# Kernel tuning notes

Measured on AMD Instinct MI355X. Metric: run time of the kernel, lower is better.

Reference implementation:

```python
import jax, jax.numpy as jnp
import numpy as np

DECAY = 0.9
BETA_OBS = 1.0
BETA_STATE = 1.0

N_OBS = 20000
N_STATES = 1024
N_ACTIONS = 64
STATE_DIM = 256
RFD = 2048


def setup_inputs() -> dict:
    key = jax.random.key(0)
    ks = jax.random.split(key, 7)
    Q = jax.random.normal(ks[0], (STATE_DIM, N_STATES), dtype=jnp.float32) / np.sqrt(STATE_DIM).astype(np.float32)
    V = jax.random.normal(ks[1], (STATE_DIM, N_ACTIONS), dtype=jnp.float32) / np.sqrt(STATE_DIM).astype(np.float32)
    W = jax.random.normal(ks[2], (RFD, STATE_DIM), dtype=jnp.float32)
    M_re = jax.random.normal(ks[3], (RFD, N_OBS), dtype=jnp.float32)
    M_im = jax.random.normal(ks[4], (RFD, N_OBS), dtype=jnp.float32)
    obs = jax.random.uniform(ks[5], (N_OBS,), dtype=jnp.float32)
    action = jax.random.uniform(ks[6], (N_ACTIONS,), dtype=jnp.float32)
    return {"Q": Q, "V": V, "W": W, "M_re": M_re, "M_im": M_im, "obs": obs, "action": action}


def reference(Q, V, W, M_re, M_im, obs, action):
    # One fused POCML step: memory write (decayed outer product), state
    # rotation via complex random-feature phase, clean_up (state-kernel
    # softmax retrieval), and obs retrieval from memory.
    D = W.shape[0]  # random_feature_dim
    M = M_re + 1j * M_im                       # [D, n_obs] complex64
    obs_c = obs.astype(jnp.complex64)
    # get_state_from_memory
    state0 = M @ obs_c                         # [D]
    # update_memory: M *= decay; M += outer(state, obs)
    M_new = DECAY * M + jnp.outer(state0, obs_c)
    # update_state: v = V @ action; phi_v = exp(1j * W @ v); state *= phi_v
    v = V @ action                             # [state_dim]
    phi_v = jnp.exp(1j * (W @ v))              # [D] complex64
    state1 = state0 * phi_v
    # clean_up: phi_Q = exp(1j * W @ Q), weights = softmax(beta*sim(phi_Q.T, state))
    phi_Q = jnp.exp(1j * (W @ Q))              # [D, n_states]
    score = BETA_STATE * (phi_Q.T @ jnp.conj(state1)).real / D  # [n_states]
    weights = jax.nn.softmax(score)
    state2 = phi_Q @ weights.astype(jnp.complex64)              # [D]
    # get_obs_from_memory: softmax(beta_obs * sim(M.T, state))
    obs_score = BETA_OBS * (M_new.T @ jnp.conj(state2)).real / D  # [n_obs]
    return jax.nn.softmax(obs_score)
```

## Files before the change

kernel.cpp:

```cpp
#include <hip/hip_runtime.h>
#include <math.h>

#define N_OBS    20000
#define N_OBS4   5000
#define N_STATES 1024
#define N_ACT    64
#define SDIM     256
#define RFD      2048
#define DECAY    0.9f

typedef float v4f __attribute__((ext_vector_type(4)));

__device__ __forceinline__ v4f ntload4(const float* p) {
    return __builtin_nontemporal_load((const v4f*)p);
}

#define OFF_SCORE  0
#define OFF_OBSACC 1024
#define ZERO_CNT   (OFF_OBSACC + N_OBS)
#define OFF_S0RE   21024
#define OFF_S0IM   23072
#define OFF_S1RE   25120
#define OFF_S1IM   27168
#define OFF_S2RE   29216
#define OFF_S2IM   31264
#define OFF_WTS    33312
#define OFF_VWS    34336
#define OFF_COSQ   34816
#define OFF_SINQ   (OFF_COSQ + RFD*N_STATES)
#define OFF_P0RE   (OFF_SINQ + RFD*N_STATES)
#define OFF_P0IM   (OFF_P0RE + 5*RFD)
#define WS_FLOATS  (OFF_P0IM + 5*RFD)

#define NB_GEMM   512
#define NB_STATE0 (5 * RFD)
#define NB_FUSED  (NB_GEMM + 1 + NB_STATE0)

__global__ __launch_bounds__(256) void k_fused(
    const float* __restrict__ Mre, const float* __restrict__ Mim,
    const float* __restrict__ obs,
    const float* __restrict__ W, const float* __restrict__ Q,
    const float* __restrict__ V, const float* __restrict__ action,
    float* __restrict__ cosQ, float* __restrict__ sinQ,
    float* __restrict__ p0re, float* __restrict__ p0im,
    float* __restrict__ vout)
{
    const int b = blockIdx.x;
    const int tid = threadIdx.x;

    if (b < NB_GEMM) {
        __shared__ float As[16][65];
        __shared__ float Bs[16][64];
        const int tx = tid & 15;
        const int ty = tid >> 4;
        const int m0 = (b >> 4) * 64;
        const int n0 = (b & 15) * 64;
        float c[4][4] = {};
        for (int k0 = 0; k0 < SDIM; k0 += 16) {
            {
                int k = tid & 15, mb = tid >> 4;
                #pragma unroll
                for (int j = 0; j < 4; j++)
                    As[k][mb + 16*j] = W[(size_t)(m0 + mb + 16*j) * SDIM + k0 + k];
            }
            {
                int n = tid & 63, kb = tid >> 6;
                #pragma unroll
                for (int j = 0; j < 4; j++)
                    Bs[kb + 4*j][n] = Q[(size_t)(k0 + kb + 4*j) * N_STATES + n0 + n];
            }
            __syncthreads();
            #pragma unroll
            for (int kk = 0; kk < 16; kk++) {
                float a[4], bb[4];
                #pragma unroll
                for (int i = 0; i < 4; i++) a[i] = As[kk][ty*4 + i];
                #pragma unroll
                for (int j = 0; j < 4; j++) bb[j] = Bs[kk][tx*4 + j];
                #pragma unroll
                for (int i = 0; i < 4; i++)
                    #pragma unroll
                    for (int j = 0; j < 4; j++)
                        c[i][j] += a[i] * bb[j];
            }
            __syncthreads();
        }
        #pragma unroll
        for (int i = 0; i < 4; i++) {
            int d = m0 + ty*4 + i;
            #pragma unroll
            for (int j = 0; j < 4; j++) {
                int s = n0 + tx*4 + j;
                float sn, cs;
                sincosf(c[i][j], &sn, &cs);
                cosQ[(size_t)d * N_STATES + s] = cs;
                sinQ[(size_t)d * N_STATES + s] = sn;
            }
        }
    } else if (b == NB_GEMM) {
        float acc = 0.f;
        for (int a = 0; a < N_ACT; a++) acc += V[tid * N_ACT + a] * action[a];
        vout[tid] = acc;
    } else {
        const int bb = b - (NB_GEMM + 1);
        const int d = bb / 5;
        const int seg = bb - d * 5;
        const float* mr = Mre + (size_t)d * N_OBS;
        const float* mi = Mim + (size_t)d * N_OBS;
        const float4* ob = (const float4*)obs;
        float ar[4] = {}, ai[4] = {};
        #pragma unroll
        for (int it = 0; it < 4; ++it) {
            int i = seg * 1024 + it * 256 + tid;
            bool ok = i < N_OBS4;
            int ic = ok ? i : 0;
            float4 o = ok ? ob[ic] : make_float4(0.f, 0.f, 0.f, 0.f);
            v4f a = ntload4(mr + 4 * (size_t)ic);
            v4f m = ntload4(mi + 4 * (size_t)ic);
            ar[it] += a.x*o.x + a.y*o.y + a.z*o.z + a.w*o.w;
            ai[it] += m.x*o.x + m.y*o.y + m.z*o.z + m.w*o.w;
        }
        float arr = (ar[0] + ar[1]) + (ar[2] + ar[3]);
        float aii = (ai[0] + ai[1]) + (ai[2] + ai[3]);
        #pragma unroll
        for (int off = 32; off > 0; off >>= 1) {
            arr += __shfl_down(arr, off);
            aii += __shfl_down(aii, off);
        }
        __shared__ float pr[4], pi[4];
        const int wave = tid >> 6, lane = tid & 63;
        if (lane == 0) { pr[wave] = arr; pi[wave] = aii; }
        __syncthreads();
        if (tid == 0) {
            p0re[seg * RFD + d] = pr[0] + pr[1] + pr[2] + pr[3];
            p0im[seg * RFD + d] = pi[0] + pi[1] + pi[2] + pi[3];
        }
    }
}

__global__ __launch_bounds__(256) void k_state1(
    const float* __restrict__ W, const float* __restrict__ vws,
    const float* __restrict__ p0re, const float* __restrict__ p0im,
    float* __restrict__ s0re, float* __restrict__ s0im,
    float* __restrict__ s1re, float* __restrict__ s1im)
{
    const int tid = threadIdx.x;
    const int w = tid >> 6, l = tid & 63;
    const int d = blockIdx.x * 4 + w;
    float4 wv = ((const float4*)(W + (size_t)d * SDIM))[l];
    float4 vv = ((const float4*)vws)[l];
    float th = wv.x*vv.x + wv.y*vv.y + wv.z*vv.z + wv.w*vv.w;
    #pragma unroll
    for (int off = 32; off > 0; off >>= 1) th += __shfl_down(th, off);
    if (l == 0) {
        float re = 0.f, im = 0.f;
        #pragma unroll
        for (int s = 0; s < 5; s++) {
            re += p0re[s * RFD + d];
            im += p0im[s * RFD + d];
        }
        s0re[d] = re; s0im[d] = im;
        float sn, cs;
        sincosf(th, &sn, &cs);
        s1re[d] = re * cs - im * sn;
        s1im[d] = re * sn + im * cs;
    }
}

__global__ __launch_bounds__(256) void k_score(
    const float* __restrict__ cosQ, const float* __restrict__ sinQ,
    const float* __restrict__ s1re, const float* __restrict__ s1im,
    float* __restrict__ score)
{
    const int s = blockIdx.x * 256 + threadIdx.x;
    const int d0 = blockIdx.y * 32;
    float acc = 0.f;
    #pragma unroll 4
    for (int j = 0; j < 32; j++) {
        int d = d0 + j;
        acc += cosQ[(size_t)d * N_STATES + s] * s1re[d]
             + sinQ[(size_t)d * N_STATES + s] * s1im[d];
    }
    atomicAdd(&score[s], acc);
}

__global__ __launch_bounds__(256) void k_softmax_w(
    const float* __restrict__ score, float* __restrict__ wts)
{
    __shared__ float red[256];
    const int tid = threadIdx.x;
    const float scale = 1.f / (float)RFD;
    float4 v = ((const float4*)score)[tid];
    v.x *= scale; v.y *= scale; v.z *= scale; v.w *= scale;
    float mx = fmaxf(fmaxf(v.x, v.y), fmaxf(v.z, v.w));
    red[tid] = mx; __syncthreads();
    for (int s = 128; s > 0; s >>= 1) {
        if (tid < s) red[tid] = fmaxf(red[tid], red[tid+s]);
        __syncthreads();
    }
    mx = red[0]; __syncthreads();
    float4 e;
    e.x = expf(v.x - mx); e.y = expf(v.y - mx);
    e.z = expf(v.z - mx); e.w = expf(v.w - mx);
    red[tid] = e.x + e.y + e.z + e.w; __syncthreads();
    for (int s = 128; s > 0; s >>= 1) {
        if (tid < s) red[tid] += red[tid+s];
        __syncthreads();
    }
    const float inv = 1.f / red[0];
    e.x *= inv; e.y *= inv; e.z *= inv; e.w *= inv;
    ((float4*)wts)[tid] = e;
}

__global__ __launch_bounds__(256) void k_state2(
    const float* __restrict__ cosQ, const float* __restrict__ sinQ,
    const float* __restrict__ wts,
    float* __restrict__ s2re, float* __restrict__ s2im)
{
    __shared__ float r1[256], r2[256];
    const int d = blockIdx.x, tid = threadIdx.x;
    float4 w = ((const float4*)wts)[tid];
    float4 a = ((const float4*)(cosQ + (size_t)d * N_STATES))[tid];
    float4 b = ((const float4*)(sinQ + (size_t)d * N_STATES))[tid];
    r1[tid] = a.x*w.x + a.y*w.y + a.z*w.z + a.w*w.w;
    r2[tid] = b.x*w.x + b.y*w.y + b.z*w.z + b.w*w.w;
    __syncthreads();
    for (int s = 128; s > 0; s >>= 1) {
        if (tid < s) { r1[tid] += r1[tid+s]; r2[tid] += r2[tid+s]; }
        __syncthreads();
    }
    if (tid == 0) { s2re[d] = r1[0]; s2im[d] = r2[0]; }
}

__global__ __launch_bounds__(256) void k_obs_acc(
    const float* __restrict__ Mre, const float* __restrict__ Mim,
    const float* __restrict__ s2re, const float* __restrict__ s2im,
    float* __restrict__ obs_acc)
{
    __shared__ float c_s[16], s_s[16];
    const int tid = threadIdx.x;
    const int dbase = blockIdx.y * 16;
    if (tid < 16) { c_s[tid] = s2re[dbase + tid]; s_s[tid] = s2im[dbase + tid]; }
    __syncthreads();
    const int idx = blockIdx.x * 256 + tid;
    if (idx < N_OBS4) {
        float4 acc[4];
        #pragma unroll
        for (int u = 0; u < 4; u++) acc[u] = make_float4(0.f, 0.f, 0.f, 0.f);
        #pragma unroll
        for (int j = 0; j < 16; j++) {
            size_t base = ((size_t)(dbase + j) * N_OBS4 + idx) * 4;
            v4f a = ntload4(Mre + base);
            v4f b = ntload4(Mim + base);
            float cc = c_s[j], ss = s_s[j];
            int u = j & 3;
            acc[u].x += a.x*cc + b.x*ss;
            acc[u].y += a.y*cc + b.y*ss;
            acc[u].z += a.z*cc + b.z*ss;
            acc[u].w += a.w*cc + b.w*ss;
        }
        float4 t;
        t.x = (acc[0].x + acc[1].x) + (acc[2].x + acc[3].x);
        t.y = (acc[0].y + acc[1].y) + (acc[2].y + acc[3].y);
        t.z = (acc[0].z + acc[1].z) + (acc[2].z + acc[3].z);
        t.w = (acc[0].w + acc[1].w) + (acc[2].w + acc[3].w);
        atomicAdd(&obs_acc[idx*4 + 0], t.x);
        atomicAdd(&obs_acc[idx*4 + 1], t.y);
        atomicAdd(&obs_acc[idx*4 + 2], t.z);
        atomicAdd(&obs_acc[idx*4 + 3], t.w);
    }
}

__global__ __launch_bounds__(1024) void k_softmax_obs(
    const float* __restrict__ obs_acc, const float* __restrict__ obs,
    const float* __restrict__ s0re, const float* __restrict__ s0im,
    const float* __restrict__ s2re, const float* __restrict__ s2im,
    float* __restrict__ out)
{
    __shared__ float red[1024];
    const int tid = threadIdx.x;
    float dp = 0.f;
    #pragma unroll
    for (int i = 0; i < 2; i++) {
        int d = tid + i * 1024;
        dp += s0re[d] * s2re[d] + s0im[d] * s2im[d];
    }
    red[tid] = dp; __syncthreads();
    for (int s = 512; s > 0; s >>= 1) {
        if (tid < s) red[tid] += red[tid+s];
        __syncthreads();
    }
    const float d0 = red[0];
    __syncthreads();
    const float scale = 1.f / (float)RFD;
    float vals[20];
    float mx = -3.402823466e+38f;
    #pragma unroll
    for (int i = 0; i < 20; i++) {
        int idx = tid + i * 1024;
        if (idx < N_OBS) {
            float sc = (DECAY * obs_acc[idx] + obs[idx] * d0) * scale;
            vals[i] = sc;
            mx = fmaxf(mx, sc);
        } else vals[i] = -3.402823466e+38f;
    }
    red[tid] = mx; __syncthreads();
    for (int s = 512; s > 0; s >>= 1) {
        if (tid < s) red[tid] = fmaxf(red[tid], red[tid+s]);
        __syncthreads();
    }
    mx = red[0]; __syncthreads();
    float sum = 0.f;
    #pragma unroll
    for (int i = 0; i < 20; i++) {
        int idx = tid + i * 1024;
        if (idx < N_OBS) {
            vals[i] = expf(vals[i] - mx);
            sum += vals[i];
        }
    }
    red[tid] = sum; __syncthreads();
    for (int s = 512; s > 0; s >>= 1) {
        if (tid < s) red[tid] += red[tid+s];
        __syncthreads();
    }
    const float inv = 1.f / red[0];
    #pragma unroll
    for (int i = 0; i < 20; i++) {
        int idx = tid + i * 1024;
        if (idx < N_OBS) out[idx] = vals[i] * inv;
    }
}

extern "C" void kernel_launch(void* const* d_in, const int* in_sizes, int n_in,
                              void* d_out, int out_size, void* d_ws, size_t ws_size,
                              hipStream_t stream) {
    const float* Q      = (const float*)d_in[0];
    const float* V      = (const float*)d_in[1];
    const float* W      = (const float*)d_in[2];
    const float* Mre    = (const float*)d_in[3];
    const float* Mim    = (const float*)d_in[4];
    const float* obs    = (const float*)d_in[5];
    const float* action = (const float*)d_in[6];
    float* out = (float*)d_out;
    float* ws  = (float*)d_ws;

    if (ws_size < (size_t)WS_FLOATS * sizeof(float)) return;

    float* score = ws + OFF_SCORE;
    float* oacc  = ws + OFF_OBSACC;
    float* s0re  = ws + OFF_S0RE;
    float* s0im  = ws + OFF_S0IM;
    float* s1re  = ws + OFF_S1RE;
    float* s1im  = ws + OFF_S1IM;
    float* s2re  = ws + OFF_S2RE;
    float* s2im  = ws + OFF_S2IM;
    float* wts   = ws + OFF_WTS;
    float* vws   = ws + OFF_VWS;
    float* cosQ  = ws + OFF_COSQ;
    float* sinQ  = ws + OFF_SINQ;
    float* p0re  = ws + OFF_P0RE;
    float* p0im  = ws + OFF_P0IM;

    hipMemsetAsync(ws, 0, (size_t)ZERO_CNT * sizeof(float), stream);

    k_fused<<<NB_FUSED, 256, 0, stream>>>(Mre, Mim, obs, W, Q, V, action,
                                          cosQ, sinQ, p0re, p0im, vws);
    k_state1<<<RFD / 4, 256, 0, stream>>>(W, vws, p0re, p0im, s0re, s0im, s1re, s1im);
    k_score<<<dim3(4, 64), 256, 0, stream>>>(cosQ, sinQ, s1re, s1im, score);
    k_softmax_w<<<1, 256, 0, stream>>>(score, wts);
    k_state2<<<RFD, 256, 0, stream>>>(cosQ, sinQ, wts, s2re, s2im);
    k_obs_acc<<<dim3((N_OBS4 + 255) / 256, RFD / 16), 256, 0, stream>>>(Mre, Mim, s2re, s2im, oacc);
    k_softmax_obs<<<1, 1024, 0, stream>>>(oacc, obs, s0re, s0im, s2re, s2im, out);
}
```

Before: 417.9 us.

## Fuse state1 into score kernel, one block per row for state0, reverse obs_acc order

```diff
diff --git a/kernel.cpp b/kernel.cpp
--- a/kernel.cpp
+++ b/kernel.cpp
@@ -11,6 +11,9 @@
 
 typedef float v4f __attribute__((ext_vector_type(4)));
 
+__device__ __forceinline__ v4f ld4(const float* p) {
+    return *(const v4f*)p;
+}
 __device__ __forceinline__ v4f ntload4(const float* p) {
     return __builtin_nontemporal_load((const v4f*)p);
 }
@@ -20,21 +23,17 @@
 #define ZERO_CNT   (OFF_OBSACC + N_OBS)
 #define OFF_S0RE   21024
 #define OFF_S0IM   23072
-#define OFF_S1RE   25120
-#define OFF_S1IM   27168
-#define OFF_S2RE   29216
-#define OFF_S2IM   31264
-#define OFF_WTS    33312
-#define OFF_VWS    34336
-#define OFF_COSQ   34816
+#define OFF_S2RE   25120
+#define OFF_S2IM   27168
+#define OFF_WTS    29216
+#define OFF_VWS    30240
+#define OFF_COSQ   30496
 #define OFF_SINQ   (OFF_COSQ + RFD*N_STATES)
-#define OFF_P0RE   (OFF_SINQ + RFD*N_STATES)
-#define OFF_P0IM   (OFF_P0RE + 5*RFD)
-#define WS_FLOATS  (OFF_P0IM + 5*RFD)
+#define WS_FLOATS  (OFF_SINQ + RFD*N_STATES)
 
 #define NB_GEMM   512
-#define NB_STATE0 (5 * RFD)
-#define NB_FUSED  (NB_GEMM + 1 + NB_STATE0)
+#define NB_P1     RFD
+#define NB_FUSED  (NB_GEMM + 1 + NB_P1)
 
 __global__ __launch_bounds__(256) void k_fused(
     const float* __restrict__ Mre, const float* __restrict__ Mim,
@@ -42,7 +41,7 @@
     const float* __restrict__ W, const float* __restrict__ Q,
     const float* __restrict__ V, const float* __restrict__ action,
     float* __restrict__ cosQ, float* __restrict__ sinQ,
-    float* __restrict__ p0re, float* __restrict__ p0im,
+    float* __restrict__ s0re, float* __restrict__ s0im,
     float* __restrict__ vout)
 {
     const int b = blockIdx.x;
@@ -102,23 +101,26 @@
         for (int a = 0; a < N_ACT; a++) acc += V[tid * N_ACT + a] * action[a];
         vout[tid] = acc;
     } else {
-        const int bb = b - (NB_GEMM + 1);
-        const int d = bb / 5;
-        const int seg = bb - d * 5;
+        const int d = b - (NB_GEMM + 1);
         const float* mr = Mre + (size_t)d * N_OBS;
         const float* mi = Mim + (size_t)d * N_OBS;
         const float4* ob = (const float4*)obs;
-        float ar[4] = {}, ai[4] = {};
-        #pragma unroll
-        for (int it = 0; it < 4; ++it) {
-            int i = seg * 1024 + it * 256 + tid;
-            bool ok = i < N_OBS4;
-            int ic = ok ? i : 0;
-            float4 o = ok ? ob[ic] : make_float4(0.f, 0.f, 0.f, 0.f);
-            v4f a = ntload4(mr + 4 * (size_t)ic);
-            v4f m = ntload4(mi + 4 * (size_t)ic);
-            ar[it] += a.x*o.x + a.y*o.y + a.z*o.z + a.w*o.w;
-            ai[it] += m.x*o.x + m.y*o.y + m.z*o.z + m.w*o.w;
+        float ar[4] = {0.f, 0.f, 0.f, 0.f}, ai[4] = {0.f, 0.f, 0.f, 0.f};
+        int i = tid;
+        #pragma unroll 4
+        for (int it = 0; it < 19; ++it, i += 256) {
+            float4 o = ob[i];
+            v4f a = ld4(mr + 4 * (size_t)i);
+            v4f m = ld4(mi + 4 * (size_t)i);
+            ar[it & 3] += a.x*o.x + a.y*o.y + a.z*o.z + a.w*o.w;
+            ai[it & 3] += m.x*o.x + m.y*o.y + m.z*o.z + m.w*o.w;
+        }
+        if (i < N_OBS4) {
+            float4 o = ob[i];
+            v4f a = ld4(mr + 4 * (size_t)i);
+            v4f m = ld4(mi + 4 * (size_t)i);
+            ar[3] += a.x*o.x + a.y*o.y + a.z*o.z + a.w*o.w;
+            ai[3] += m.x*o.x + m.y*o.y + m.z*o.z + m.w*o.w;
         }
         float arr = (ar[0] + ar[1]) + (ar[2] + ar[3]);
         float aii = (ai[0] + ai[1]) + (ai[2] + ai[3]);
@@ -132,54 +134,50 @@
         if (lane == 0) { pr[wave] = arr; pi[wave] = aii; }
         __syncthreads();
         if (tid == 0) {
-            p0re[seg * RFD + d] = pr[0] + pr[1] + pr[2] + pr[3];
-            p0im[seg * RFD + d] = pi[0] + pi[1] + pi[2] + pi[3];
-        }
-    }
-}
-
-__global__ __launch_bounds__(256) void k_state1(
-    const float* __restrict__ W, const float* __restrict__ vws,
-    const float* __restrict__ p0re, const float* __restrict__ p0im,
-    float* __restrict__ s0re, float* __restrict__ s0im,
-    float* __restrict__ s1re, float* __restrict__ s1im)
-{
-    const int tid = threadIdx.x;
-    const int w = tid >> 6, l = tid & 63;
-    const int d = blockIdx.x * 4 + w;
-    float4 wv = ((const float4*)(W + (size_t)d * SDIM))[l];
-    float4 vv = ((const float4*)vws)[l];
-    float th = wv.x*vv.x + wv.y*vv.y + wv.z*vv.z + wv.w*vv.w;
-    #pragma unroll
-    for (int off = 32; off > 0; off >>= 1) th += __shfl_down(th, off);
-    if (l == 0) {
-        float re = 0.f, im = 0.f;
-        #pragma unroll
-        for (int s = 0; s < 5; s++) {
-            re += p0re[s * RFD + d];
-            im += p0im[s * RFD + d];
-        }
-        s0re[d] = re; s0im[d] = im;
-        float sn, cs;
-        sincosf(th, &sn, &cs);
-        s1re[d] = re * cs - im * sn;
-        s1im[d] = re * sn + im * cs;
+            s0re[d] = pr[0] + pr[1] + pr[2] + pr[3];
+            s0im[d] = pi[0] + pi[1] + pi[2] + pi[3];
+        }
     }
 }
 
 __global__ __launch_bounds__(256) void k_score(
     const float* __restrict__ cosQ, const float* __restrict__ sinQ,
-    const float* __restrict__ s1re, const float* __restrict__ s1im,
+    const float* __restrict__ W, const float* __restrict__ vws,
+    const float* __restrict__ s0re, const float* __restrict__ s0im,
     float* __restrict__ score)
 {
-    const int s = blockIdx.x * 256 + threadIdx.x;
+    __shared__ float s1r_s[32], s1i_s[32];
+    const int tid = threadIdx.x;
     const int d0 = blockIdx.y * 32;
+    {
+        const int r = tid >> 3, g = tid & 7;
+        const float4* wv4 = (const float4*)(W + (size_t)(d0 + r) * SDIM + g * 32);
+        const float4* vv4 = (const float4*)(vws + g * 32);
+        float th = 0.f;
+        #pragma unroll
+        for (int j = 0; j < 8; j++) {
+            float4 wv = wv4[j], vv = vv4[j];
+            th += wv.x*vv.x + wv.y*vv.y + wv.z*vv.z + wv.w*vv.w;
+        }
+        th += __shfl_xor(th, 4);
+        th += __shfl_xor(th, 2);
+        th += __shfl_xor(th, 1);
+        if (g == 0) {
+            float sn, cs;
+            sincosf(th, &sn, &cs);
+            float re = s0re[d0 + r], im = s0im[d0 + r];
+            s1r_s[r] = re * cs - im * sn;
+            s1i_s[r] = re * sn + im * cs;
+        }
+    }
+    __syncthreads();
+    const int s = blockIdx.x * 256 + tid;
     float acc = 0.f;
     #pragma unroll 4
     for (int j = 0; j < 32; j++) {
         int d = d0 + j;
-        acc += cosQ[(size_t)d * N_STATES + s] * s1re[d]
-             + sinQ[(size_t)d * N_STATES + s] * s1im[d];
+        acc += cosQ[(size_t)d * N_STATES + s] * s1r_s[j]
+             + sinQ[(size_t)d * N_STATES + s] * s1i_s[j];
     }
     atomicAdd(&score[s], acc);
 }
@@ -237,38 +235,36 @@
     const float* __restrict__ s2re, const float* __restrict__ s2im,
     float* __restrict__ obs_acc)
 {
-    __shared__ float c_s[16], s_s[16];
-    const int tid = threadIdx.x;
-    const int dbase = blockIdx.y * 16;
-    if (tid < 16) { c_s[tid] = s2re[dbase + tid]; s_s[tid] = s2im[dbase + tid]; }
+    __shared__ float c_s[64], s_s[64];
+    const int tid = threadIdx.x;
+    const int dbase = (31 - (int)blockIdx.y) * 64;
+    if (tid < 64) { c_s[tid] = s2re[dbase + tid]; s_s[tid] = s2im[dbase + tid]; }
     __syncthreads();
     const int idx = blockIdx.x * 256 + tid;
-    if (idx < N_OBS4) {
-        float4 acc[4];
-        #pragma unroll
-        for (int u = 0; u < 4; u++) acc[u] = make_float4(0.f, 0.f, 0.f, 0.f);
-        #pragma unroll
-        for (int j = 0; j < 16; j++) {
-            size_t base = ((size_t)(dbase + j) * N_OBS4 + idx) * 4;
-            v4f a = ntload4(Mre + base);
-            v4f b = ntload4(Mim + base);
-            float cc = c_s[j], ss = s_s[j];
-            int u = j & 3;
-            acc[u].x += a.x*cc + b.x*ss;
-            acc[u].y += a.y*cc + b.y*ss;
-            acc[u].z += a.z*cc + b.z*ss;
-            acc[u].w += a.w*cc + b.w*ss;
-        }
-        float4 t;
-        t.x = (acc[0].x + acc[1].x) + (acc[2].x + acc[3].x);
-        t.y = (acc[0].y + acc[1].y) + (acc[2].y + acc[3].y);
-        t.z = (acc[0].z + acc[1].z) + (acc[2].z + acc[3].z);
-        t.w = (acc[0].w + acc[1].w) + (acc[2].w + acc[3].w);
-        atomicAdd(&obs_acc[idx*4 + 0], t.x);
-        atomicAdd(&obs_acc[idx*4 + 1], t.y);
-        atomicAdd(&obs_acc[idx*4 + 2], t.z);
-        atomicAdd(&obs_acc[idx*4 + 3], t.w);
-    }
+    if (idx >= N_OBS4) return;
+    float4 acc[4];
+    #pragma unroll
+    for (int u = 0; u < 4; u++) acc[u] = make_float4(0.f, 0.f, 0.f, 0.f);
+    #pragma unroll 8
+    for (int j = 0; j < 64; j++) {
+        size_t base = ((size_t)(dbase + j) * N_OBS4 + idx) * 4;
+        v4f a = ntload4(Mre + base);
+        v4f b = ntload4(Mim + base);
+        float cc = c_s[j], ss = s_s[j];
+        acc[j & 3].x += a.x*cc + b.x*ss;
+        acc[j & 3].y += a.y*cc + b.y*ss;
+        acc[j & 3].z += a.z*cc + b.z*ss;
+        acc[j & 3].w += a.w*cc + b.w*ss;
+    }
+    float4 t;
+    t.x = (acc[0].x + acc[1].x) + (acc[2].x + acc[3].x);
+    t.y = (acc[0].y + acc[1].y) + (acc[2].y + acc[3].y);
+    t.z = (acc[0].z + acc[1].z) + (acc[2].z + acc[3].z);
+    t.w = (acc[0].w + acc[1].w) + (acc[2].w + acc[3].w);
+    atomicAdd(&obs_acc[idx*4 + 0], t.x);
+    atomicAdd(&obs_acc[idx*4 + 1], t.y);
+    atomicAdd(&obs_acc[idx*4 + 2], t.z);
+    atomicAdd(&obs_acc[idx*4 + 3], t.w);
 }
 
 __global__ __launch_bounds__(1024) void k_softmax_obs(
@@ -351,25 +347,20 @@
     float* oacc  = ws + OFF_OBSACC;
     float* s0re  = ws + OFF_S0RE;
     float* s0im  = ws + OFF_S0IM;
-    float* s1re  = ws + OFF_S1RE;
-    float* s1im  = ws + OFF_S1IM;
     float* s2re  = ws + OFF_S2RE;
     float* s2im  = ws + OFF_S2IM;
     float* wts   = ws + OFF_WTS;
     float* vws   = ws + OFF_VWS;
     float* cosQ  = ws + OFF_COSQ;
     float* sinQ  = ws + OFF_SINQ;
-    float* p0re  = ws + OFF_P0RE;
-    float* p0im  = ws + OFF_P0IM;
 
     hipMemsetAsync(ws, 0, (size_t)ZERO_CNT * sizeof(float), stream);
 
     k_fused<<<NB_FUSED, 256, 0, stream>>>(Mre, Mim, obs, W, Q, V, action,
-                                          cosQ, sinQ, p0re, p0im, vws);
-    k_state1<<<RFD / 4, 256, 0, stream>>>(W, vws, p0re, p0im, s0re, s0im, s1re, s1im);
-    k_score<<<dim3(4, 64), 256, 0, stream>>>(cosQ, sinQ, s1re, s1im, score);
+                                          cosQ, sinQ, s0re, s0im, vws);
+    k_score<<<dim3(4, 64), 256, 0, stream>>>(cosQ, sinQ, W, vws, s0re, s0im, score);
     k_softmax_w<<<1, 256, 0, stream>>>(score, wts);
     k_state2<<<RFD, 256, 0, stream>>>(cosQ, sinQ, wts, s2re, s2im);
-    k_obs_acc<<<dim3((N_OBS4 + 255) / 256, RFD / 16), 256, 0, stream>>>(Mre, Mim, s2re, s2im, oacc);
+    k_obs_acc<<<dim3(20, 32), 256, 0, stream>>>(Mre, Mim, s2re, s2im, oacc);
     k_softmax_obs<<<1, 1024, 0, stream>>>(oacc, obs, s0re, s0im, s2re, s2im, out);
 }
```

Result: no change. 421.8 us (+0.9%).
